# Kernel tuning notes

Measured on AMD Instinct MI355X. Metric: run time of the kernel, lower is better.

Reference implementation:

```python
import jax, jax.numpy as jnp
import numpy as np

D = 1024
M = 8
K = 256
BZ = 32768
ALPHA = 10.0
EPS = 1e-12


def setup_inputs() -> dict:
    key = jax.random.key(0)
    k1, k2 = jax.random.split(key)
    x = jax.random.normal(k1, (BZ, D), dtype=jnp.float32)
    c = jax.random.normal(k2, (D, K), dtype=jnp.float32)
    return {"x": x, "c": c}


def reference(x, c):
    bz, d = x.shape
    L = d // M  # sub-vector length = 128
    # [bz, M, L]: split into M sub-spaces, L2-normalize each sample's sub-vector
    xs = x.reshape(bz, M, L)
    xs = xs / jnp.maximum(jnp.linalg.norm(xs, axis=-1, keepdims=True), EPS)
    # codebook per sub-space: [M, L, K]
    cs = c.reshape(M, L, K)
    # scaled similarity logits [bz, M, K]
    logits = (2.0 * ALPHA) * jnp.einsum("bml,mlk->bmk", xs, cs)
    w = jax.nn.softmax(logits, axis=-1)
    # soft reconstruction back into each sub-space: [bz, M, L]
    out = jnp.einsum("bmk,mlk->bml", w, cs)
    return out.reshape(bz, d)
```

## Files before the change

kernel.cpp:

```cpp
#include <hip/hip_runtime.h>


#define D_  1024
#define K_  256
#define L_  128

typedef _Float16 f16;
typedef f16 f16x8 __attribute__((ext_vector_type(8)));
typedef f16 f16x4 __attribute__((ext_vector_type(4)));
typedef float f32x4 __attribute__((ext_vector_type(4)));
typedef unsigned int u32;

__global__ __launch_bounds__(128)
void pqn_prep(const float* __restrict__ c, f16* __restrict__ ws) {
    const int b   = blockIdx.x;
    const int m   = b >> 8;
    const int cc  = b & 255;
    const int l   = threadIdx.x;
    const int rho = (cc & ~31) | ((cc & 4) << 2) | ((cc & 24) >> 1) | (cc & 3);
    float v = c[(size_t)(m * L_ + l) * K_ + cc];
    ws[((size_t)m * K_ + rho) * L_ + l] = (f16)v;
}

__global__ __launch_bounds__(1024)
void pqn_main(const float* __restrict__ x, const float* __restrict__ c,
              const f16* __restrict__ ws, float* __restrict__ out) {
    __shared__ unsigned char lds[131072];
    unsigned char* csA = lds;
    unsigned char* csB = lds + 65536;

    const int tid  = threadIdx.x;
    const int m    = blockIdx.x >> 5;
    const int bm   = blockIdx.x & 31;
    const int lane = tid & 63;
    const int w    = tid >> 6;
    const int n    = lane & 15;
    const int g    = lane >> 4;

    {
        const f16* wsm0 = ws + (size_t)m * (K_ * L_);
        #pragma unroll
        for (int i = 0; i < 4; ++i) {
            int idx = i * 1024 + tid;
            int r   = idx >> 4;
            int q   = idx & 15;
            f16x8 v = *reinterpret_cast<const f16x8*>(wsm0 + (size_t)idx * 8);
            *reinterpret_cast<f16x8*>(csA + r * 256 + ((q * 16) ^ ((r & 7) << 4))) = v;
        }
    }
    const float* cm = c + (size_t)m * L_ * K_;
    {
        const int R0 = tid >> 6;
        const int f  = tid & 63;
        #pragma unroll
        for (int b = 0; b < 4; ++b) {
            int R  = b * 16 + R0;
            int l0 = 2 * R;
            float4 a  = *reinterpret_cast<const float4*>(cm + (size_t)l0 * K_ + 4 * f);
            float4 bb = *reinterpret_cast<const float4*>(cm + (size_t)(l0 + 1) * K_ + 4 * f);
            f16x4 va = {(f16)a.x, (f16)a.y, (f16)a.z, (f16)a.w};
            f16x4 vb = {(f16)bb.x, (f16)bb.y, (f16)bb.z, (f16)bb.w};
            *reinterpret_cast<f16x4*>(csB + l0 * 512       + ((8 * f) ^ ((l0 & 7) << 4))) = va;
            *reinterpret_cast<f16x4*>(csB + (l0 + 1) * 512 + ((8 * f) ^ (((l0 + 1) & 7) << 4))) = vb;
        }
    }
    __syncthreads();

    #pragma unroll 1
    for (int it = 0; it < 4; ++it) {
        const int row0 = bm * 1024 + it * 256 + w * 16 + n;

        const float* px = x + (size_t)row0 * D_ + m * L_ + 8 * g;
        float ss = 0.f;
        f16x8 bf[4];
        #pragma unroll
        for (int ks = 0; ks < 4; ++ks) {
            float4 lo = *reinterpret_cast<const float4*>(px + 32 * ks);
            float4 hi = *reinterpret_cast<const float4*>(px + 32 * ks + 4);
            ss = fmaf(lo.x, lo.x, ss); ss = fmaf(lo.y, lo.y, ss);
            ss = fmaf(lo.z, lo.z, ss); ss = fmaf(lo.w, lo.w, ss);
            ss = fmaf(hi.x, hi.x, ss); ss = fmaf(hi.y, hi.y, ss);
            ss = fmaf(hi.z, hi.z, ss); ss = fmaf(hi.w, hi.w, ss);
            bf[ks][0] = (f16)lo.x; bf[ks][1] = (f16)lo.y;
            bf[ks][2] = (f16)lo.z; bf[ks][3] = (f16)lo.w;
            bf[ks][4] = (f16)hi.x; bf[ks][5] = (f16)hi.y;
            bf[ks][6] = (f16)hi.z; bf[ks][7] = (f16)hi.w;
        }
        ss += __shfl_xor(ss, 16);
        ss += __shfl_xor(ss, 32);
        const float fac = 20.0f / fmaxf(sqrtf(ss), 1e-12f);

        f32x4 acc2[8];
        const f32x4 fzero = {0.f, 0.f, 0.f, 0.f};
        #pragma unroll
        for (int lt = 0; lt < 8; ++lt) acc2[lt] = fzero;
        float mrun = -3.0e38f;
        float sp   = 0.f;

        #pragma unroll 1
        for (int a = 0; a < 4; ++a) {
            f32x4 acc[4];
            #pragma unroll
            for (int ct = 0; ct < 4; ++ct) acc[ct] = fzero;
            #pragma unroll
            for (int ks = 0; ks < 4; ++ks) {
                #pragma unroll
                for (int ct = 0; ct < 4; ++ct) {
                    f16x8 af = *reinterpret_cast<const f16x8*>(
                        csA + (a * 64 + ct * 16 + n) * 256 +
                        ((64 * ks + 16 * g) ^ ((n & 7) << 4)));
                    acc[ct] = __builtin_amdgcn_mfma_f32_16x16x32_f16(af, bf[ks], acc[ct], 0, 0, 0);
                }
            }
            __builtin_amdgcn_sched_barrier(0);

            float cmax = -3.0e38f;
            #pragma unroll
            for (int ct = 0; ct < 4; ++ct) {
                acc[ct][0] *= fac; acc[ct][1] *= fac;
                acc[ct][2] *= fac; acc[ct][3] *= fac;
                cmax = fmaxf(cmax, fmaxf(fmaxf(acc[ct][0], acc[ct][1]),
                                         fmaxf(acc[ct][2], acc[ct][3])));
            }
            cmax = fmaxf(cmax, __shfl_xor(cmax, 16));
            cmax = fmaxf(cmax, __shfl_xor(cmax, 32));
            const float mnew = fmaxf(mrun, cmax);
            const float r = __expf(mrun - mnew);
            mrun = mnew;
            sp *= r;
            #pragma unroll
            for (int lt = 0; lt < 8; ++lt) {
                acc2[lt][0] *= r; acc2[lt][1] *= r;
                acc2[lt][2] *= r; acc2[lt][3] *= r;
            }
            u32 P[8];
            #pragma unroll
            for (int ct = 0; ct < 4; ++ct) {
                float p0 = __expf(acc[ct][0] - mrun);
                float p1 = __expf(acc[ct][1] - mrun);
                float p2 = __expf(acc[ct][2] - mrun);
                float p3 = __expf(acc[ct][3] - mrun);
                sp += (p0 + p1) + (p2 + p3);
                P[2 * ct]     = __builtin_bit_cast(u32, __builtin_amdgcn_cvt_pkrtz(p0, p1));
                P[2 * ct + 1] = __builtin_bit_cast(u32, __builtin_amdgcn_cvt_pkrtz(p2, p3));
            }
            #pragma unroll
            for (int j = 0; j < 2; ++j) {
                union { f16x8 v; u32 q[4]; } pb;
                pb.q[0] = P[4 * j + 0]; pb.q[1] = P[4 * j + 1];
                pb.q[2] = P[4 * j + 2]; pb.q[3] = P[4 * j + 3];
                const int ks2 = 2 * a + j;
                #pragma unroll
                for (int lt = 0; lt < 8; ++lt) {
                    f16x8 a2 = *reinterpret_cast<const f16x8*>(
                        csB + (lt * 16 + n) * 512 + ((64 * ks2 + 16 * g) ^ ((n & 7) << 4)));
                    acc2[lt] = __builtin_amdgcn_mfma_f32_16x16x32_f16(a2, pb.v, acc2[lt], 0, 0, 0);
                }
            }
            __builtin_amdgcn_sched_barrier(0);
        }

        sp += __shfl_xor(sp, 16);
        sp += __shfl_xor(sp, 32);
        const float invS = 1.0f / sp;

        float* po = out + (size_t)row0 * D_ + m * L_ + 4 * g;
        #pragma unroll
        for (int lt = 0; lt < 8; ++lt) {
            f32x4 v;
            v[0] = acc2[lt][0] * invS; v[1] = acc2[lt][1] * invS;
            v[2] = acc2[lt][2] * invS; v[3] = acc2[lt][3] * invS;
            *reinterpret_cast<f32x4*>(po + 16 * lt) = v;
        }
    }
}

extern "C" void kernel_launch(void* const* d_in, const int* in_sizes, int n_in,
                              void* d_out, int out_size, void* d_ws, size_t ws_size,
                              hipStream_t stream) {
    const float* x = (const float*)d_in[0];
    const float* c = (const float*)d_in[1];
    float* out = (float*)d_out;
    f16* ws = (f16*)d_ws;
    (void)in_sizes; (void)n_in; (void)out_size; (void)ws_size;

    pqn_prep<<<dim3(2048), dim3(128), 0, stream>>>(c, ws);
    pqn_main<<<dim3(256), dim3(1024), 0, stream>>>(x, c, ws, out);
}
```

Measured before the change: 69.64 us.

## Keep half of codebook A fragments in registers and skip small softmax rescales

Result: slower. 160.4 us (+130.3%).

```diff
diff --git a/kernel.cpp b/kernel.cpp
--- a/kernel.cpp
+++ b/kernel.cpp
@@ -22,12 +22,66 @@
     ws[((size_t)m * K_ + rho) * L_ + l] = (f16)v;
 }
 
+#define CHUNK_TAIL(ACC, KS2B)                                                  \
+    {                                                                          \
+        float cmax = -3.0e38f;                                                 \
+        _Pragma("unroll")                                                      \
+        for (int ct = 0; ct < 4; ++ct) {                                       \
+            ACC[ct][0] *= fac; ACC[ct][1] *= fac;                              \
+            ACC[ct][2] *= fac; ACC[ct][3] *= fac;                              \
+            cmax = fmaxf(cmax, fmaxf(fmaxf(ACC[ct][0], ACC[ct][1]),            \
+                                     fmaxf(ACC[ct][2], ACC[ct][3])));          \
+        }                                                                      \
+        cmax = fmaxf(cmax, __shfl_xor(cmax, 16));                              \
+        cmax = fmaxf(cmax, __shfl_xor(cmax, 32));                              \
+        if (!__all(cmax <= mrun + 8.0f)) {                                     \
+            const float mnew = fmaxf(mrun, cmax);                              \
+            const float r = __expf(mrun - mnew);                               \
+            mrun = mnew;                                                       \
+            sp *= r;                                                           \
+            _Pragma("unroll")                                                  \
+            for (int lt = 0; lt < 8; ++lt) {                                   \
+                acc2[lt][0] *= r; acc2[lt][1] *= r;                            \
+                acc2[lt][2] *= r; acc2[lt][3] *= r;                            \
+            }                                                                  \
+        }                                                                      \
+        u32 P[8];                                                              \
+        _Pragma("unroll")                                                      \
+        for (int ct = 0; ct < 4; ++ct) {                                       \
+            float p0 = __expf(ACC[ct][0] - mrun);                              \
+            float p1 = __expf(ACC[ct][1] - mrun);                              \
+            float p2 = __expf(ACC[ct][2] - mrun);                              \
+            float p3 = __expf(ACC[ct][3] - mrun);                              \
+            sp += (p0 + p1) + (p2 + p3);                                       \
+            P[2 * ct]     = __builtin_bit_cast(u32,                            \
+                __builtin_amdgcn_cvt_pkrtz(p0, p1));                           \
+            P[2 * ct + 1] = __builtin_bit_cast(u32,                            \
+                __builtin_amdgcn_cvt_pkrtz(p2, p3));                           \
+        }                                                                      \
+        _Pragma("unroll")                                                      \
+        for (int j = 0; j < 2; ++j) {                                          \
+            union { f16x8 v; u32 q[4]; } pb;                                   \
+            pb.q[0] = P[4 * j + 0]; pb.q[1] = P[4 * j + 1];                    \
+            pb.q[2] = P[4 * j + 2]; pb.q[3] = P[4 * j + 3];                    \
+            const int ks2 = (KS2B) + j;                                        \
+            _Pragma("unroll")                                                  \
+            for (int lt = 0; lt < 8; ++lt) {                                   \
+                f16x8 a2 = *reinterpret_cast<const f16x8*>(                    \
+                    csB + (lt * 16 + n) * 512 +                                \
+                    ((64 * ks2 + 16 * g) ^ ((n & 7) << 4)));                   \
+                acc2[lt] = __builtin_amdgcn_mfma_f32_16x16x32_f16(             \
+                    a2, pb.v, acc2[lt], 0, 0, 0);                              \
+            }                                                                  \
+        }                                                                      \
+        __builtin_amdgcn_sched_barrier(0);                                     \
+    }
+
 __global__ __launch_bounds__(1024)
 void pqn_main(const float* __restrict__ x, const float* __restrict__ c,
               const f16* __restrict__ ws, float* __restrict__ out) {
-    __shared__ unsigned char lds[131072];
+    __shared__ unsigned char lds[98304];
     unsigned char* csA = lds;
-    unsigned char* csB = lds + 65536;
+    unsigned char* csB = lds + 32768;
 
     const int tid  = threadIdx.x;
     const int m    = blockIdx.x >> 5;
@@ -38,14 +92,14 @@
     const int g    = lane >> 4;
 
     {
-        const f16* wsm0 = ws + (size_t)m * (K_ * L_);
-        #pragma unroll
-        for (int i = 0; i < 4; ++i) {
+        const f16* wsm0 = ws + (size_t)m * (K_ * L_) + (size_t)128 * L_;
+        #pragma unroll
+        for (int i = 0; i < 2; ++i) {
             int idx = i * 1024 + tid;
-            int r   = idx >> 4;
+            int rr  = idx >> 4;
             int q   = idx & 15;
             f16x8 v = *reinterpret_cast<const f16x8*>(wsm0 + (size_t)idx * 8);
-            *reinterpret_cast<f16x8*>(csA + r * 256 + ((q * 16) ^ ((r & 7) << 4))) = v;
+            *reinterpret_cast<f16x8*>(csA + rr * 256 + ((q * 16) ^ ((rr & 7) << 4))) = v;
         }
     }
     const float* cm = c + (size_t)m * L_ * K_;
@@ -64,6 +118,18 @@
             *reinterpret_cast<f16x4*>(csB + (l0 + 1) * 512 + ((8 * f) ^ (((l0 + 1) & 7) << 4))) = vb;
         }
     }
+
+    const f16* wsm = ws + (size_t)m * (K_ * L_) + (size_t)n * L_ + 8 * g;
+    f16x8 FA[2][4][4];
+    #pragma unroll
+    for (int a = 0; a < 2; ++a)
+        #pragma unroll
+        for (int ct = 0; ct < 4; ++ct)
+            #pragma unroll
+            for (int ks = 0; ks < 4; ++ks)
+                FA[a][ct][ks] = *reinterpret_cast<const f16x8*>(
+                    wsm + (a * 64 + ct * 16) * L_ + 32 * ks);
+
     __syncthreads();
 
     #pragma unroll 1
@@ -97,8 +163,23 @@
         float mrun = -3.0e38f;
         float sp   = 0.f;
 
+        #pragma unroll
+        for (int a = 0; a < 2; ++a) {
+            f32x4 acc[4];
+            #pragma unroll
+            for (int ct = 0; ct < 4; ++ct) acc[ct] = fzero;
+            #pragma unroll
+            for (int ks = 0; ks < 4; ++ks)
+                #pragma unroll
+                for (int ct = 0; ct < 4; ++ct)
+                    acc[ct] = __builtin_amdgcn_mfma_f32_16x16x32_f16(
+                        FA[a][ct][ks], bf[ks], acc[ct], 0, 0, 0);
+            __builtin_amdgcn_sched_barrier(0);
+            CHUNK_TAIL(acc, 2 * a)
+        }
+
         #pragma unroll 1
-        for (int a = 0; a < 4; ++a) {
+        for (int aa = 0; aa < 2; ++aa) {
             f32x4 acc[4];
             #pragma unroll
             for (int ct = 0; ct < 4; ++ct) acc[ct] = fzero;
@@ -107,57 +188,13 @@
                 #pragma unroll
                 for (int ct = 0; ct < 4; ++ct) {
                     f16x8 af = *reinterpret_cast<const f16x8*>(
-                        csA + (a * 64 + ct * 16 + n) * 256 +
+                        csA + (aa * 64 + ct * 16 + n) * 256 +
                         ((64 * ks + 16 * g) ^ ((n & 7) << 4)));
                     acc[ct] = __builtin_amdgcn_mfma_f32_16x16x32_f16(af, bf[ks], acc[ct], 0, 0, 0);
                 }
             }
             __builtin_amdgcn_sched_barrier(0);
-
-            float cmax = -3.0e38f;
-            #pragma unroll
-            for (int ct = 0; ct < 4; ++ct) {
-                acc[ct][0] *= fac; acc[ct][1] *= fac;
-                acc[ct][2] *= fac; acc[ct][3] *= fac;
-                cmax = fmaxf(cmax, fmaxf(fmaxf(acc[ct][0], acc[ct][1]),
-                                         fmaxf(acc[ct][2], acc[ct][3])));
-            }
-            cmax = fmaxf(cmax, __shfl_xor(cmax, 16));
-            cmax = fmaxf(cmax, __shfl_xor(cmax, 32));
-            const float mnew = fmaxf(mrun, cmax);
-            const float r = __expf(mrun - mnew);
-            mrun = mnew;
-            sp *= r;
-            #pragma unroll
-            for (int lt = 0; lt < 8; ++lt) {
-                acc2[lt][0] *= r; acc2[lt][1] *= r;
-                acc2[lt][2] *= r; acc2[lt][3] *= r;
-            }
-            u32 P[8];
-            #pragma unroll
-            for (int ct = 0; ct < 4; ++ct) {
-                float p0 = __expf(acc[ct][0] - mrun);
-                float p1 = __expf(acc[ct][1] - mrun);
-                float p2 = __expf(acc[ct][2] - mrun);
-                float p3 = __expf(acc[ct][3] - mrun);
-                sp += (p0 + p1) + (p2 + p3);
-                P[2 * ct]     = __builtin_bit_cast(u32, __builtin_amdgcn_cvt_pkrtz(p0, p1));
-                P[2 * ct + 1] = __builtin_bit_cast(u32, __builtin_amdgcn_cvt_pkrtz(p2, p3));
-            }
-            #pragma unroll
-            for (int j = 0; j < 2; ++j) {
-                union { f16x8 v; u32 q[4]; } pb;
-                pb.q[0] = P[4 * j + 0]; pb.q[1] = P[4 * j + 1];
-                pb.q[2] = P[4 * j + 2]; pb.q[3] = P[4 * j + 3];
-                const int ks2 = 2 * a + j;
-                #pragma unroll
-                for (int lt = 0; lt < 8; ++lt) {
-                    f16x8 a2 = *reinterpret_cast<const f16x8*>(
-                        csB + (lt * 16 + n) * 512 + ((64 * ks2 + 16 * g) ^ ((n & 7) << 4)));
-                    acc2[lt] = __builtin_amdgcn_mfma_f32_16x16x32_f16(a2, pb.v, acc2[lt], 0, 0, 0);
-                }
-            }
-            __builtin_amdgcn_sched_barrier(0);
+            CHUNK_TAIL(acc, 4 + 2 * aa)
         }
 
         sp += __shfl_xor(sp, 16);
```
